# Performance work log

Measured on AMD Instinct MI355X. Metric: run time of the kernel, lower is better.

Reference implementation:

```python
import jax, jax.numpy as jnp
import numpy as np

# ---- config (mirrors init_kwargs) ----
T = 1024          # num tokens (one causal sequence)
H = 1024          # hidden_size
NQ, NK, D = 16, 4, 64   # q heads, kv heads, head_dim (GQA)
I_DENSE = 4096    # dense FFN intermediate
I_MOE = 512       # expert FFN intermediate
E, K = 8, 2       # num_experts, top_k
EPS = 1e-6
THETA = 10000.0


def setup_inputs() -> dict:
    key = jax.random.key(0)
    ks = jax.random.split(key, 20)
    rn = lambda k, shp: (jax.random.normal(k, shp, dtype=jnp.float32) * 0.02)
    QKV = (NQ + 2 * NK) * D
    return {
        "hidden_states": jax.random.normal(ks[0], (T, H), dtype=jnp.float32),
        "residual": jax.random.normal(ks[1], (T, H), dtype=jnp.float32),
        "positions": jnp.arange(T, dtype=jnp.int32),
        "ln0_w": jnp.ones((H,), jnp.float32),
        "pa0_w": jnp.ones((H,), jnp.float32),
        "ln1_w": jnp.ones((H,), jnp.float32),
        "pa1_w": jnp.ones((H,), jnp.float32),
        # attention weights (stored [in, out] so x @ W)
        "qkv0_w": rn(ks[2], (H, QKV)),
        "o0_w": rn(ks[3], (NQ * D, H)),
        "qkv1_w": rn(ks[4], (H, QKV)),
        "o1_w": rn(ks[5], (NQ * D, H)),
        # dense MLPs (merged gate_up: first half gate, second half up)
        "gu0_w": rn(ks[6], (H, 2 * I_DENSE)),
        "dn0_w": rn(ks[7], (I_DENSE, H)),
        "gu1_w": rn(ks[8], (H, 2 * I_DENSE)),
        "dn1_w": rn(ks[9], (I_DENSE, H)),
        # MoE: router gate + per-expert SwiGLU weights
        "gate_w": rn(ks[10], (H, E)),
        "w13": rn(ks[11], (E, H, 2 * I_MOE)),
        "w2": rn(ks[12], (E, I_MOE, H)),
    }


def _rmsnorm(x, w):
    v = jnp.mean(jnp.square(x.astype(jnp.float32)), axis=-1, keepdims=True)
    return (x.astype(jnp.float32) * jax.lax.rsqrt(v + EPS)).astype(x.dtype) * w


def _add_rmsnorm(x, res, w):
    # sglang fused add + RMSNorm: residual <- x + residual; out <- rmsnorm(residual)
    res = x + res
    return _rmsnorm(res, w), res


def _rope(pos, x):
    # neox-style rotary over full head_dim; x: [T, n_heads, D]
    half = D // 2
    inv_freq = 1.0 / (THETA ** (jnp.arange(half, dtype=jnp.float32) / half))
    f = pos.astype(jnp.float32)[:, None] * inv_freq            # [T, half]
    cos, sin = jnp.cos(f)[:, None, :], jnp.sin(f)[:, None, :]  # [T, 1, half]
    x1, x2 = x[..., :half], x[..., half:]
    return jnp.concatenate([x1 * cos - x2 * sin, x2 * cos + x1 * sin], axis=-1)


def _attention(pos, x, qkv_w, o_w):
    qkv = x @ qkv_w
    q = qkv[:, : NQ * D].reshape(T, NQ, D)
    k = qkv[:, NQ * D : (NQ + NK) * D].reshape(T, NK, D)
    v = qkv[:, (NQ + NK) * D :].reshape(T, NK, D)
    q, k = _rope(pos, q), _rope(pos, k)
    g = NQ // NK
    qg = q.reshape(T, NK, g, D)
    scores = jnp.einsum("tkgd,skd->kgts", qg, k) * (D ** -0.5)  # [NK,g,T,T]
    causal = jnp.tril(jnp.ones((T, T), bool))
    scores = jnp.where(causal, scores, jnp.float32(-1e30))
    p = jax.nn.softmax(scores, axis=-1)
    o = jnp.einsum("kgts,skd->tkgd", p, v).reshape(T, NQ * D)
    return o @ o_w


def _dense_mlp(x, gu_w, dn_w):
    gu = x @ gu_w
    h = jax.nn.silu(gu[:, :I_DENSE]) * gu[:, I_DENSE:]  # SiluAndMul
    return h @ dn_w


def _moe(x, gate_w, w13, w2):
    # router in fp32 (router_dtype == 'float32'), softmax, top-k, no renormalize
    logits = x.astype(jnp.float32) @ gate_w.astype(jnp.float32)  # [T, E]
    probs = jax.nn.softmax(logits, axis=-1)
    topw, topi = jax.lax.top_k(probs, K)                         # [T, K]
    rows = jnp.arange(x.shape[0])[:, None]
    combine = jnp.zeros((x.shape[0], E), jnp.float32).at[rows, topi].set(topw)
    combine = combine.astype(x.dtype)
    out = jnp.zeros_like(x)
    for e in range(E):  # fixed small expert count: grouped-GEMM reference
        g = x @ w13[e]
        h = jax.nn.silu(g[:, :I_MOE]) * g[:, I_MOE:]
        out = out + combine[:, e : e + 1] * (h @ w2[e])
    return out


def reference(hidden_states, residual, positions, ln0_w, pa0_w, ln1_w, pa1_w,
              qkv0_w, o0_w, qkv1_w, o1_w, gu0_w, dn0_w, gu1_w, dn1_w,
              gate_w, w13, w2):
    h, r = _add_rmsnorm(hidden_states, residual, ln0_w)
    h = _attention(positions, h, qkv0_w, o0_w)
    h, r = _add_rmsnorm(h, r, pa0_w)
    shortcut = _moe(h, gate_w, w13, w2)      # MoE runs on the shortcut branch
    h = _dense_mlp(h, gu0_w, dn0_w)
    h, r = _add_rmsnorm(h, r, ln1_w)
    h = _attention(positions, h, qkv1_w, o1_w)
    h, r = _add_rmsnorm(h, r, pa1_w)
    h = _dense_mlp(h, gu1_w, dn1_w)
    h = h + shortcut                          # combine shortcut MoE output
    return h, r
```

## Files before the change

kernel.cpp:

```cpp
#include <hip/hip_runtime.h>
#include <math.h>

namespace {

constexpr int kT = 1024;
constexpr int kH = 1024;
constexpr int kNQ = 16;
constexpr int kNKV = 4;
constexpr int kD = 64;
constexpr int kQKV = (kNQ + 2 * kNKV) * kD;
constexpr int kIDense = 4096;
constexpr int kIMoe = 512;
constexpr int kE = 8;
constexpr float kEps = 1e-6f;
constexpr long kTH = (long)kT * kH;

typedef __attribute__((ext_vector_type(8))) short short8;
typedef __attribute__((ext_vector_type(4))) float f32x4;

__device__ __forceinline__ ushort f2bf(float f) {
    union { float f; uint32_t u; } v; v.f = f;
    uint32_t r = (v.u + 0x7fffu + ((v.u >> 16) & 1u)) >> 16;
    return (ushort)r;
}
__device__ __forceinline__ void gload16(const void* g, void* l) {
    __builtin_amdgcn_global_load_lds(
        (const __attribute__((address_space(1))) void*)g,
        (__attribute__((address_space(3))) void*)l, 16, 0, 0);
}

__global__ __launch_bounds__(256) void add_rmsnorm_kernel(
    const float* __restrict__ xP, int nparts, const float* __restrict__ res,
    const float* __restrict__ w, float* __restrict__ h32,
    ushort* __restrict__ h16, float* __restrict__ r_out)
{
    __shared__ float red[4];
    const int t = blockIdx.x;
    const int i = threadIdx.x;
    const size_t base = (size_t)t * kH;
    float4 s = reinterpret_cast<const float4*>(res + base)[i];
    for (int p = 0; p < nparts; p++) {
        float4 a = reinterpret_cast<const float4*>(xP + p * kTH + base)[i];
        s.x += a.x; s.y += a.y; s.z += a.z; s.w += a.w;
    }
    reinterpret_cast<float4*>(r_out + base)[i] = s;
    float ss = s.x * s.x + s.y * s.y + s.z * s.z + s.w * s.w;
    #pragma unroll
    for (int off = 32; off > 0; off >>= 1) ss += __shfl_down(ss, off);
    if ((i & 63) == 0) red[i >> 6] = ss;
    __syncthreads();
    const float tot = red[0] + red[1] + red[2] + red[3];
    const float inv = rsqrtf(tot * (1.0f / kH) + kEps);
    float4 wv = reinterpret_cast<const float4*>(w)[i];
    float4 o = make_float4(s.x * inv * wv.x, s.y * inv * wv.y,
                           s.z * inv * wv.z, s.w * inv * wv.w);
    reinterpret_cast<float4*>(h32 + base)[i] = o;
    ushort4 u;
    u.x = f2bf(o.x); u.y = f2bf(o.y); u.z = f2bf(o.z); u.w = f2bf(o.w);
    reinterpret_cast<ushort4*>(h16 + base)[i] = u;
}

__global__ __launch_bounds__(256) void transpose_bf16_kernel(
    const float* __restrict__ W, ushort* __restrict__ WT,
    int R, int Cn, int ld_w, long w_z_stride, long wt_z_stride)
{
    __shared__ float tile[64 * 65];
    const int z = blockIdx.z;
    const float* Wz = W + (size_t)z * w_z_stride;
    ushort* WTz = WT + (size_t)z * wt_z_stride;
    const int r0 = blockIdx.y * 64;
    const int c0 = blockIdx.x * 64;
    const int tid = threadIdx.x;
    const int lr = tid >> 4;
    const int lc = (tid & 15) * 4;
    #pragma unroll
    for (int p = 0; p < 4; p++) {
        const int row = p * 16 + lr;
        float4 v = *reinterpret_cast<const float4*>(
            &Wz[(size_t)(r0 + row) * ld_w + c0 + lc]);
        tile[row * 65 + lc + 0] = v.x;
        tile[row * 65 + lc + 1] = v.y;
        tile[row * 65 + lc + 2] = v.z;
        tile[row * 65 + lc + 3] = v.w;
    }
    __syncthreads();
    const int ocl = tid >> 2;
    const int q = tid & 3;
    ushort u[16];
    #pragma unroll
    for (int e = 0; e < 16; e++)
        u[e] = f2bf(tile[(q * 16 + e) * 65 + ocl]);
    ushort* dst = &WTz[(size_t)(c0 + ocl) * R + r0 + q * 16];
    *reinterpret_cast<short8*>(dst) = *reinterpret_cast<short8*>(&u[0]);
    *reinterpret_cast<short8*>(dst + 8) = *reinterpret_cast<short8*>(&u[8]);
}

template <bool GATED>
__global__ __launch_bounds__(256) void mgemm_kernel(
    const ushort* __restrict__ A, const ushort* __restrict__ B,
    float* __restrict__ Cf, ushort* __restrict__ C16,
    const float* __restrict__ scale,
    int lda, int ldb, int ldc, int kc,
    int gate_off_rows, long b_z_stride, int c_z_col, int k_z_off,
    int scale_stride, long c_fstride)
{
    __shared__ __align__(16) ushort As[64 * 64];
    __shared__ __align__(16) ushort Bs[64 * 64];
    __shared__ __align__(16) ushort Us[GATED ? 64 * 64 : 8];

    const int z = blockIdx.z;
    const int gy = gridDim.y;
    const int nf = gridDim.x * gy;
    const int fid = blockIdx.x + gridDim.x * blockIdx.y;
    const int qq = nf >> 3;
    const int id2 = (fid & 7) * qq + (fid >> 3);
    const int m0 = (id2 % gy) * 64;
    const int n0 = (id2 / gy) * 64;

    const int tid = threadIdx.x;
    const ushort* Bz = B + (size_t)z * b_z_stride;
    const int k0 = z * k_z_off;

    const int arow = tid >> 3;
    const int achk = tid & 7;

    const int lane = tid & 63;
    const int wave = tid >> 6;
    const int wr = (wave >> 1) * 32;
    const int wc = (wave & 1) * 32;
    const int lrow = lane & 15;
    const int lg = lane >> 4;

    f32x4 accg[2][2] = {};
    f32x4 accu[2][2] = {};

    for (int kk0 = 0; kk0 < kc; kk0 += 64) {
        const int kbase = k0 + kk0;
        #pragma unroll
        for (int c = 0; c < 2; c++) {
            const int row = c * 32 + arow;
            const int cs = (achk + (row & 7)) & 7;
            gload16(A + (size_t)(m0 + row) * lda + kbase + cs * 8,
                    (char*)As + c * 4096 + tid * 16);
            gload16(Bz + (size_t)(n0 + row) * ldb + kbase + cs * 8,
                    (char*)Bs + c * 4096 + tid * 16);
            if constexpr (GATED)
                gload16(Bz + (size_t)(gate_off_rows + n0 + row) * ldb + kbase + cs * 8,
                        (char*)Us + c * 4096 + tid * 16);
        }
        __syncthreads();

        short8 af[2][2], bfr[2][2];
        #pragma unroll
        for (int mf = 0; mf < 2; mf++)
            #pragma unroll
            for (int kk = 0; kk < 2; kk++) {
                const int r = wr + mf * 16 + lrow;
                const int sl = ((kk * 4 + lg) - (r & 7)) & 7;
                af[mf][kk] = *reinterpret_cast<const short8*>(
                    (const char*)As + r * 128 + sl * 16);
            }
        #pragma unroll
        for (int nf2 = 0; nf2 < 2; nf2++)
            #pragma unroll
            for (int kk = 0; kk < 2; kk++) {
                const int n = wc + nf2 * 16 + lrow;
                const int sl = ((kk * 4 + lg) - (n & 7)) & 7;
                bfr[nf2][kk] = *reinterpret_cast<const short8*>(
                    (const char*)Bs + n * 128 + sl * 16);
            }
        #pragma unroll
        for (int mf = 0; mf < 2; mf++)
            #pragma unroll
            for (int nf2 = 0; nf2 < 2; nf2++)
                #pragma unroll
                for (int kk = 0; kk < 2; kk++)
                    accg[mf][nf2] = __builtin_amdgcn_mfma_f32_16x16x32_bf16(
                        af[mf][kk], bfr[nf2][kk], accg[mf][nf2], 0, 0, 0);
        if constexpr (GATED) {
            short8 uf[2][2];
            #pragma unroll
            for (int nf2 = 0; nf2 < 2; nf2++)
                #pragma unroll
                for (int kk = 0; kk < 2; kk++) {
                    const int n = wc + nf2 * 16 + lrow;
                    const int sl = ((kk * 4 + lg) - (n & 7)) & 7;
                    uf[nf2][kk] = *reinterpret_cast<const short8*>(
                        (const char*)Us + n * 128 + sl * 16);
                }
            #pragma unroll
            for (int mf = 0; mf < 2; mf++)
                #pragma unroll
                for (int nf2 = 0; nf2 < 2; nf2++)
                    #pragma unroll
                    for (int kk = 0; kk < 2; kk++)
                        accu[mf][nf2] = __builtin_amdgcn_mfma_f32_16x16x32_bf16(
                            af[mf][kk], uf[nf2][kk], accu[mf][nf2], 0, 0, 0);
        }
        __syncthreads();
    }

    const int r4 = (lane >> 4) * 4;
    const int cl = lane & 15;
    const int ccol = z * c_z_col;
    float* Cfz = Cf ? Cf + (size_t)z * c_fstride : nullptr;
    #pragma unroll
    for (int mf = 0; mf < 2; mf++) {
        #pragma unroll
        for (int nf2 = 0; nf2 < 2; nf2++) {
            #pragma unroll
            for (int j = 0; j < 4; j++) {
                const int row = m0 + wr + mf * 16 + r4 + j;
                const int col = ccol + n0 + wc + nf2 * 16 + cl;
                if constexpr (GATED) {
                    const float g = accg[mf][nf2][j];
                    const float u = accu[mf][nf2][j];
                    const float sv =
                        scale ? scale[(size_t)row * scale_stride + z] : 1.0f;
                    const float h = (g / (1.0f + __expf(-g))) * u * sv;
                    C16[(size_t)row * ldc + col] = f2bf(h);
                } else {
                    Cfz[(size_t)row * ldc + col] = accg[mf][nf2][j];
                }
            }
        }
    }
}

__global__ __launch_bounds__(256) void rope_pack_kernel(
    const float* __restrict__ qkv, const int* __restrict__ positions,
    ushort* __restrict__ Qb, ushort* __restrict__ Kb)
{
    const int t = blockIdx.x;
    const float pos = (float)positions[t];
    for (int item = threadIdx.x; item < (kNQ + kNKV) * 32; item += 256) {
        const int head = item >> 5;
        const int i = item & 31;
        const float inv_freq = powf(10000.0f, -(float)i * (1.0f / 32.0f));
        const float f = pos * inv_freq;
        float sv, cv;
        sincosf(f, &sv, &cv);
        const size_t off = (size_t)t * kQKV + head * kD;
        const float x1 = qkv[off + i];
        const float x2 = qkv[off + 32 + i];
        const float r1 = x1 * cv - x2 * sv;
        const float r2 = x2 * cv + x1 * sv;
        if (head < kNQ) {
            ushort* q = Qb + ((size_t)head * kT + t) * kD;
            q[i] = f2bf(r1 * 0.125f);
            q[i + 32] = f2bf(r2 * 0.125f);
        } else {
            ushort* k = Kb + ((size_t)(head - kNQ) * kT + t) * kD;
            k[i] = f2bf(r1);
            k[i + 32] = f2bf(r2);
        }
    }
}

__global__ __launch_bounds__(64) void gate_topk_kernel(
    const float* __restrict__ h, const float* __restrict__ gate_w,
    float* __restrict__ combine)
{
    const int t = blockIdx.x;
    const int lane = threadIdx.x;
    float acc[kE] = {};
    for (int i = lane; i < kH; i += 64) {
        const float xv = h[(size_t)t * kH + i];
        const float* gw = gate_w + (size_t)i * kE;
        #pragma unroll
        for (int e = 0; e < kE; e++) acc[e] += xv * gw[e];
    }
    #pragma unroll
    for (int e = 0; e < kE; e++) {
        #pragma unroll
        for (int off = 32; off > 0; off >>= 1) acc[e] += __shfl_down(acc[e], off);
    }
    if (lane == 0) {
        float mx = acc[0];
        #pragma unroll
        for (int e = 1; e < kE; e++) mx = fmaxf(mx, acc[e]);
        float p[kE];
        float s = 0.0f;
        #pragma unroll
        for (int e = 0; e < kE; e++) { p[e] = expf(acc[e] - mx); s += p[e]; }
        const float invs = 1.0f / s;
        #pragma unroll
        for (int e = 0; e < kE; e++) p[e] *= invs;
        int i1 = 0;
        #pragma unroll
        for (int e = 1; e < kE; e++) if (p[e] > p[i1]) i1 = e;
        int i2 = (i1 == 0) ? 1 : 0;
        #pragma unroll
        for (int e = 0; e < kE; e++) if (e != i1 && p[e] > p[i2]) i2 = e;
        float outv[kE];
        #pragma unroll
        for (int e = 0; e < kE; e++) outv[e] = 0.0f;
        outv[i1] = p[i1];
        outv[i2] = p[i2];
        #pragma unroll
        for (int e = 0; e < kE; e++) combine[(size_t)t * kE + e] = outv[e];
    }
}

__global__ __launch_bounds__(256) void attn_mfma_kernel(
    const ushort* __restrict__ Qb, const ushort* __restrict__ Kb,
    const ushort* __restrict__ Vt, float* __restrict__ Opart,
    float* __restrict__ mlpart)
{
    __shared__ __align__(16) ushort Qs[64 * 64];
    __shared__ __align__(16) ushort Ks[64 * 64];
    __shared__ __align__(16) ushort Vs[64 * 64];
    __shared__ __align__(16) ushort Ps[64 * 64];
    const int tid = threadIdx.x;
    const int qbi = (int)gridDim.x - 1 - blockIdx.x;
    const int qb = qbi * 64;
    const int hq = blockIdx.y;
    const int zp = blockIdx.z;
    const int kvh = hq >> 2;

    const int nt = qbi + 1;
    const int halfc = (nt + 1) >> 1;
    const int sbeg = zp ? halfc : 0;
    const int send = zp ? nt : halfc;

    float* Oz = Opart + (((size_t)zp * kNQ + hq) * kT + qb) * kD;
    float* mlz = mlpart + (((size_t)zp * kNQ + hq) * kT + qb) * 2;

    if (sbeg >= send) {
        for (int i = tid; i < 64 * kD; i += 256) Oz[(i >> 6) * kD + (i & 63)] = 0.f;
        for (int i = tid; i < 64; i += 256) { mlz[i * 2] = -1e30f; mlz[i * 2 + 1] = 0.f; }
        return;
    }

    const int lane = tid & 63;
    const int wave = tid >> 6;
    const int lrow = lane & 15;
    const int g = lane >> 4;
    const int srow = tid >> 3;
    const int sx = tid & 7;
    const ushort* Qg = Qb + ((size_t)hq * kT + qb) * kD;
    const ushort* Kg = Kb + (size_t)kvh * kT * kD;
    const ushort* Vg = Vt + (size_t)kvh * kD * kT;
    const int xr = (lrow & 7) << 4;

    #pragma unroll
    for (int c = 0; c < 2; c++) {
        const int row = c * 32 + srow;
        gload16(Qg + (size_t)row * kD + ((sx ^ (row & 7)) * 8),
                (char*)Qs + c * 4096 + tid * 16);
    }
    __syncthreads();
    short8 qf[2];
    #pragma unroll
    for (int kk = 0; kk < 2; kk++)
        qf[kk] = *reinterpret_cast<const short8*>(
            (const char*)Qs + (16 * wave + lrow) * 128 + ((kk * 64 + g * 16) ^ xr));

    f32x4 oacc[4] = {};
    float mrow = -1e30f, lsum = 0.0f;

    for (int ti = sbeg; ti < send; ++ti) {
        const int s0 = ti * 64;
        __syncthreads();
        #pragma unroll
        for (int c = 0; c < 2; c++) {
            const int row = c * 32 + srow;
            gload16(Kg + (size_t)(s0 + row) * kD + ((sx ^ (row & 7)) * 8),
                    (char*)Ks + c * 4096 + tid * 16);
            gload16(Vg + (size_t)row * kT + s0 + ((sx ^ (row & 7)) * 8),
                    (char*)Vs + c * 4096 + tid * 16);
        }
        __syncthreads();

        f32x4 sacc[4] = {};
        #pragma unroll
        for (int nf = 0; nf < 4; nf++) {
            #pragma unroll
            for (int kk = 0; kk < 2; kk++) {
                short8 kf = *reinterpret_cast<const short8*>(
                    (const char*)Ks + (nf * 16 + lrow) * 128 + ((kk * 64 + g * 16) ^ xr));
                sacc[nf] = __builtin_amdgcn_mfma_f32_16x16x32_bf16(
                    kf, qf[kk], sacc[nf], 0, 0, 0);
            }
        }

        const bool diag = (s0 == qb);
        float pv[16];
        float mloc = -1e30f;
        #pragma unroll
        for (int nf = 0; nf < 4; nf++)
            #pragma unroll
            for (int j = 0; j < 4; j++) {
                float s = sacc[nf][j];
                if (diag && (nf * 16 + g * 4 + j > 16 * wave + lrow)) s = -1e30f;
                pv[nf * 4 + j] = s;
                mloc = fmaxf(mloc, s);
            }
        mloc = fmaxf(mloc, __shfl_xor(mloc, 16));
        mloc = fmaxf(mloc, __shfl_xor(mloc, 32));
        const float mnew = fmaxf(mrow, mloc);
        const float alpha = __expf(mrow - mnew);
        float psum = 0.0f;
        #pragma unroll
        for (int j = 0; j < 16; j++) { pv[j] = __expf(pv[j] - mnew); psum += pv[j]; }
        psum += __shfl_xor(psum, 16);
        psum += __shfl_xor(psum, 32);
        lsum = lsum * alpha + psum;
        mrow = mnew;

        const int prow = 16 * wave + lrow;
        #pragma unroll
        for (int nf = 0; nf < 4; nf++)
            #pragma unroll
            for (int jp = 0; jp < 2; jp++) {
                uint32_t pk = (uint32_t)f2bf(pv[nf * 4 + jp * 2]) |
                              ((uint32_t)f2bf(pv[nf * 4 + jp * 2 + 1]) << 16);
                *reinterpret_cast<uint32_t*>(
                    (char*)Ps + prow * 128 + ((nf * 32 + g * 8 + jp * 4) ^ xr)) = pk;
            }

        float aj[4];
        #pragma unroll
        for (int j = 0; j < 4; j++) aj[j] = __shfl(alpha, g * 4 + j);
        #pragma unroll
        for (int nf = 0; nf < 4; nf++)
            #pragma unroll
            for (int j = 0; j < 4; j++) oacc[nf][j] *= aj[j];

        short8 paf[2];
        #pragma unroll
        for (int kk = 0; kk < 2; kk++)
            paf[kk] = *reinterpret_cast<const short8*>(
                (const char*)Ps + prow * 128 + ((kk * 64 + g * 16) ^ xr));
        #pragma unroll
        for (int nf = 0; nf < 4; nf++)
            #pragma unroll
            for (int kk = 0; kk < 2; kk++) {
                short8 vf = *reinterpret_cast<const short8*>(
                    (const char*)Vs + (nf * 16 + lrow) * 128 + ((kk * 64 + g * 16) ^ xr));
                oacc[nf] = __builtin_amdgcn_mfma_f32_16x16x32_bf16(
                    paf[kk], vf, oacc[nf], 0, 0, 0);
            }
    }

    #pragma unroll
    for (int nf = 0; nf < 4; nf++)
        #pragma unroll
        for (int j = 0; j < 4; j++)
            Oz[(16 * wave + g * 4 + j) * kD + nf * 16 + lrow] = oacc[nf][j];
    if (g == 0) {
        mlz[(16 * wave + lrow) * 2 + 0] = mrow;
        mlz[(16 * wave + lrow) * 2 + 1] = lsum;
    }
}

__global__ __launch_bounds__(256) void attn_merge_kernel(
    const float* __restrict__ Opart, const float* __restrict__ mlpart,
    ushort* __restrict__ attn_o)
{
    const int trow = blockIdx.x;
    const int tid = threadIdx.x;
    const int head = tid >> 4;
    const int c4 = (tid & 15) * 4;
    const size_t i0 = ((size_t)head * kT + trow);
    const size_t i1 = (((size_t)kNQ + head) * kT + trow);
    const float m0 = mlpart[i0 * 2], l0 = mlpart[i0 * 2 + 1];
    const float m1 = mlpart[i1 * 2], l1 = mlpart[i1 * 2 + 1];
    const float m = fmaxf(m0, m1);
    const float e0 = __expf(m0 - m), e1 = __expf(m1 - m);
    const float inv = 1.0f / (l0 * e0 + l1 * e1);
    float4 a = *reinterpret_cast<const float4*>(&Opart[i0 * kD + c4]);
    float4 b = *reinterpret_cast<const float4*>(&Opart[i1 * kD + c4]);
    ushort4 u;
    u.x = f2bf((a.x * e0 + b.x * e1) * inv);
    u.y = f2bf((a.y * e0 + b.y * e1) * inv);
    u.z = f2bf((a.z * e0 + b.z * e1) * inv);
    u.w = f2bf((a.w * e0 + b.w * e1) * inv);
    *reinterpret_cast<ushort4*>(
        &attn_o[(size_t)trow * (kNQ * kD) + head * kD + c4]) = u;
}

__global__ __launch_bounds__(256) void final_out_kernel(
    const float* __restrict__ mlpP, const float* __restrict__ scP,
    const float* __restrict__ r, float* __restrict__ out)
{
    const int i = blockIdx.x * 256 + threadIdx.x;
    float4 s = make_float4(0.f, 0.f, 0.f, 0.f);
    #pragma unroll
    for (int p = 0; p < 4; p++) {
        float4 a = reinterpret_cast<const float4*>(mlpP + p * kTH)[i];
        float4 b = reinterpret_cast<const float4*>(scP + p * kTH)[i];
        s.x += a.x + b.x; s.y += a.y + b.y; s.z += a.z + b.z; s.w += a.w + b.w;
    }
    reinterpret_cast<float4*>(out)[i] = s;
    reinterpret_cast<float4*>(out + kTH)[i] =
        reinterpret_cast<const float4*>(r)[i];
}

}

extern "C" void kernel_launch(void* const* d_in, const int* in_sizes, int n_in,
                              void* d_out, int out_size, void* d_ws, size_t ws_size,
                              hipStream_t stream) {
    (void)in_sizes; (void)n_in; (void)out_size; (void)ws_size;
    const float* hidden   = (const float*)d_in[0];
    const float* residual = (const float*)d_in[1];
    const int*   positions= (const int*)d_in[2];
    const float* ln0_w    = (const float*)d_in[3];
    const float* pa0_w    = (const float*)d_in[4];
    const float* ln1_w    = (const float*)d_in[5];
    const float* pa1_w    = (const float*)d_in[6];
    const float* qkv0_w   = (const float*)d_in[7];
    const float* o0_w     = (const float*)d_in[8];
    const float* qkv1_w   = (const float*)d_in[9];
    const float* o1_w     = (const float*)d_in[10];
    const float* gu0_w    = (const float*)d_in[11];
    const float* dn0_w    = (const float*)d_in[12];
    const float* gu1_w    = (const float*)d_in[13];
    const float* dn1_w    = (const float*)d_in[14];
    const float* gate_w   = (const float*)d_in[15];
    const float* w13      = (const float*)d_in[16];
    const float* w2       = (const float*)d_in[17];
    float* out_h = (float*)d_out;

    char* wsb = (char*)d_ws;
    float*  r_buf   = (float*)(wsb + (0ull  << 20));
    float*  h32     = (float*)(wsb + (4ull  << 20));
    float*  t0P     = (float*)(wsb + (8ull  << 20));
    float*  cb_buf  = (float*)(wsb + (8ull  << 20));
    float*  Opart   = (float*)(wsb + (16ull << 20));
    float*  scP     = (float*)(wsb + (24ull << 20));
    ushort* h16     = (ushort*)(wsb + (40ull << 20));
    ushort* ao16    = (ushort*)(wsb + (42ull << 20));
    float*  qkv_buf = (float*)(wsb + (44ull << 20));
    ushort* he16    = (ushort*)(wsb + (44ull << 20));
    float*  ml_buf  = (float*)(wsb + (50ull << 20));
    ushort* wT      = (ushort*)(wsb + (52ull << 20));
    ushort* Qb      = (ushort*)(wsb + (62ull << 20));
    ushort* Kb      = (ushort*)(wsb + (64ull << 20));
    ushort* VtG     = (ushort*)(wsb + (65ull << 20));

    auto transp = [&](const float* W, int R, int Cn, int nz, long zs_in, long zs_out) {
        transpose_bf16_kernel<<<dim3(Cn / 64, R / 64, nz), 256, 0, stream>>>(
            W, wT, R, Cn, Cn, zs_in, zs_out);
    };
    auto gemm_f32 = [&](const ushort* A, float* C, int N, int lda_,
                        int ldb_, int ldc_, int nz, int kc, int kzoff) {
        mgemm_kernel<false><<<dim3(N / 64, kT / 64, nz), 256, 0, stream>>>(
            A, wT, C, nullptr, nullptr, lda_, ldb_, ldc_, kc,
            0, 0, 0, kzoff, 0, kTH);
    };
    auto attention = [&](const float* qkv_w, const float* o_w) {
        transp(qkv_w, kH, kQKV, 1, 0, 0);
        mgemm_kernel<false><<<dim3(kQKV / 64, kT / 64, 1), 256, 0, stream>>>(
            h16, wT, qkv_buf, nullptr, nullptr, kH, kH, kQKV, kH,
            0, 0, 0, 0, 0, 0);
        rope_pack_kernel<<<kT, 256, 0, stream>>>(qkv_buf, positions, Qb, Kb);
        transpose_bf16_kernel<<<dim3(1, kT / 64, kNKV), 256, 0, stream>>>(
            qkv_buf + (kNQ + kNKV) * kD, VtG, kT, kD, kQKV, kD, (long)kD * kT);
        attn_mfma_kernel<<<dim3(kT / 64, kNQ, 2), 256, 0, stream>>>(
            Qb, Kb, VtG, Opart, ml_buf);
        attn_merge_kernel<<<kT, 256, 0, stream>>>(Opart, ml_buf, ao16);
        transp(o_w, kNQ * kD, kH, 1, 0, 0);
        gemm_f32(ao16, t0P, kH, kNQ * kD, kNQ * kD, kH, 2, 512, 512);
    };
    auto dense_mlp = [&](const float* gu_w, const float* dn_w) {
        transp(gu_w, kH, 2 * kIDense, 1, 0, 0);
        mgemm_kernel<true><<<dim3(kIDense / 64, kT / 64, 1), 256, 0, stream>>>(
            h16, wT, nullptr, he16, nullptr, kH, kH, kIDense, kH,
            kIDense, 0, 0, 0, 0, 0);
        transp(dn_w, kIDense, kH, 1, 0, 0);
        gemm_f32(he16, t0P, kH, kIDense, kIDense, kH, 4, 1024, 1024);
    };

    add_rmsnorm_kernel<<<kT, 256, 0, stream>>>(hidden, 1, residual, ln0_w, h32, h16, r_buf);
    attention(qkv0_w, o0_w);
    add_rmsnorm_kernel<<<kT, 256, 0, stream>>>(t0P, 2, r_buf, pa0_w, h32, h16, r_buf);
    gate_topk_kernel<<<kT, 64, 0, stream>>>(h32, gate_w, cb_buf);
    transp(w13, kH, 2 * kIMoe, kE, (long)kH * 2 * kIMoe, (long)kH * 2 * kIMoe);
    mgemm_kernel<true><<<dim3(kIMoe / 64, kT / 64, kE), 256, 0, stream>>>(
        h16, wT, nullptr, he16, cb_buf, kH, kH, kIDense, kH,
        kIMoe, (long)kH * 2 * kIMoe, kIMoe, 0, kE, 0);
    transp(w2, kE * kIMoe, kH, 1, 0, 0);
    gemm_f32(he16, scP, kH, kIDense, kIDense, kH, 4, 1024, 1024);
    dense_mlp(gu0_w, dn0_w);
    add_rmsnorm_kernel<<<kT, 256, 0, stream>>>(t0P, 4, r_buf, ln1_w, h32, h16, r_buf);
    attention(qkv1_w, o1_w);
    add_rmsnorm_kernel<<<kT, 256, 0, stream>>>(t0P, 2, r_buf, pa1_w, h32, h16, r_buf);
    dense_mlp(gu1_w, dn1_w);
    final_out_kernel<<<(kT * kH / 4) / 256, 256, 0, stream>>>(t0P, scP, r_buf, out_h);
}
```

Before: 335.8 us.

## Widen GEMM tiles to 64x128 with 512 threads and fuse router into RMSNorm

Replaces the 64x64 MFMA GEMM with a 64x128 tile variant run by 8 waves, so each A tile loaded into LDS is reused across twice as many output columns and the block count halves. Separately, the MoE router logits, softmax and top-2 selection are folded into the post-attention add+RMSNorm kernel, removing one launch and a reread of the normalized activations. The larger tile doubles LDS use per block and reduces grid size, which may cut occupancy on small GEMMs such as the MoE ones.

```diff
diff --git a/kernel.cpp b/kernel.cpp
--- a/kernel.cpp
+++ b/kernel.cpp
@@ -32,9 +32,11 @@
 __global__ __launch_bounds__(256) void add_rmsnorm_kernel(
     const float* __restrict__ xP, int nparts, const float* __restrict__ res,
     const float* __restrict__ w, float* __restrict__ h32,
-    ushort* __restrict__ h16, float* __restrict__ r_out)
+    ushort* __restrict__ h16, float* __restrict__ r_out,
+    const float* __restrict__ gate_w, float* __restrict__ combine)
 {
     __shared__ float red[4];
+    __shared__ float gred[4][kE];
     const int t = blockIdx.x;
     const int i = threadIdx.x;
     const size_t base = (size_t)t * kH;
@@ -58,6 +60,51 @@
     ushort4 u;
     u.x = f2bf(o.x); u.y = f2bf(o.y); u.z = f2bf(o.z); u.w = f2bf(o.w);
     reinterpret_cast<ushort4*>(h16 + base)[i] = u;
+
+    if (gate_w != nullptr) {
+        float le[kE];
+        const float* gw = gate_w + (size_t)(i * 4) * kE;
+        #pragma unroll
+        for (int e = 0; e < kE; e++)
+            le[e] = o.x * gw[e] + o.y * gw[kE + e] +
+                    o.z * gw[2 * kE + e] + o.w * gw[3 * kE + e];
+        #pragma unroll
+        for (int e = 0; e < kE; e++) {
+            #pragma unroll
+            for (int off = 32; off > 0; off >>= 1)
+                le[e] += __shfl_down(le[e], off);
+        }
+        if ((i & 63) == 0) {
+            #pragma unroll
+            for (int e = 0; e < kE; e++) gred[i >> 6][e] = le[e];
+        }
+        __syncthreads();
+        if (i == 0) {
+            float p[kE];
+            float mx = -1e30f;
+            #pragma unroll
+            for (int e = 0; e < kE; e++) {
+                p[e] = gred[0][e] + gred[1][e] + gred[2][e] + gred[3][e];
+                mx = fmaxf(mx, p[e]);
+            }
+            float sum = 0.0f;
+            #pragma unroll
+            for (int e = 0; e < kE; e++) { p[e] = __expf(p[e] - mx); sum += p[e]; }
+            const float invs = 1.0f / sum;
+            #pragma unroll
+            for (int e = 0; e < kE; e++) p[e] *= invs;
+            int i1 = 0;
+            #pragma unroll
+            for (int e = 1; e < kE; e++) if (p[e] > p[i1]) i1 = e;
+            int i2 = (i1 == 0) ? 1 : 0;
+            #pragma unroll
+            for (int e = 0; e < kE; e++) if (e != i1 && p[e] > p[i2]) i2 = e;
+            #pragma unroll
+            for (int e = 0; e < kE; e++)
+                combine[(size_t)t * kE + e] =
+                    (e == i1) ? p[i1] : (e == i2) ? p[i2] : 0.0f;
+        }
+    }
 }
 
 __global__ __launch_bounds__(256) void transpose_bf16_kernel(
@@ -96,7 +143,7 @@
 }
 
 template <bool GATED>
-__global__ __launch_bounds__(256) void mgemm_kernel(
+__global__ __launch_bounds__(512) void mgemm128_kernel(
     const ushort* __restrict__ A, const ushort* __restrict__ B,
     float* __restrict__ Cf, ushort* __restrict__ C16,
     const float* __restrict__ scale,
@@ -105,8 +152,8 @@
     int scale_stride, long c_fstride)
 {
     __shared__ __align__(16) ushort As[64 * 64];
-    __shared__ __align__(16) ushort Bs[64 * 64];
-    __shared__ __align__(16) ushort Us[GATED ? 64 * 64 : 8];
+    __shared__ __align__(16) ushort Bs[128 * 64];
+    __shared__ __align__(16) ushort Us[GATED ? 128 * 64 : 8];
 
     const int z = blockIdx.z;
     const int gy = gridDim.y;
@@ -115,19 +162,19 @@
     const int qq = nf >> 3;
     const int id2 = (fid & 7) * qq + (fid >> 3);
     const int m0 = (id2 % gy) * 64;
-    const int n0 = (id2 / gy) * 64;
+    const int n0 = (id2 / gy) * 128;
 
     const int tid = threadIdx.x;
     const ushort* Bz = B + (size_t)z * b_z_stride;
     const int k0 = z * k_z_off;
 
-    const int arow = tid >> 3;
-    const int achk = tid & 7;
+    const int sr = tid >> 3;
+    const int sc = tid & 7;
 
     const int lane = tid & 63;
     const int wave = tid >> 6;
-    const int wr = (wave >> 1) * 32;
-    const int wc = (wave & 1) * 32;
+    const int wr = (wave >> 2) * 32;
+    const int wc = (wave & 3) * 32;
     const int lrow = lane & 15;
     const int lg = lane >> 4;
 
@@ -136,17 +183,20 @@
 
     for (int kk0 = 0; kk0 < kc; kk0 += 64) {
         const int kbase = k0 + kk0;
+        {
+            const int csA = (sc + (sr & 7)) & 7;
+            gload16(A + (size_t)(m0 + sr) * lda + kbase + csA * 8,
+                    (char*)As + tid * 16);
+        }
         #pragma unroll
         for (int c = 0; c < 2; c++) {
-            const int row = c * 32 + arow;
-            const int cs = (achk + (row & 7)) & 7;
-            gload16(A + (size_t)(m0 + row) * lda + kbase + cs * 8,
-                    (char*)As + c * 4096 + tid * 16);
+            const int row = c * 64 + sr;
+            const int cs = (sc + (row & 7)) & 7;
             gload16(Bz + (size_t)(n0 + row) * ldb + kbase + cs * 8,
-                    (char*)Bs + c * 4096 + tid * 16);
+                    (char*)Bs + c * 8192 + tid * 16);
             if constexpr (GATED)
                 gload16(Bz + (size_t)(gate_off_rows + n0 + row) * ldb + kbase + cs * 8,
-                        (char*)Us + c * 4096 + tid * 16);
+                        (char*)Us + c * 8192 + tid * 16);
         }
         __syncthreads();
 
@@ -257,51 +307,6 @@
     }
 }
 
-__global__ __launch_bounds__(64) void gate_topk_kernel(
-    const float* __restrict__ h, const float* __restrict__ gate_w,
-    float* __restrict__ combine)
-{
-    const int t = blockIdx.x;
-    const int lane = threadIdx.x;
-    float acc[kE] = {};
-    for (int i = lane; i < kH; i += 64) {
-        const float xv = h[(size_t)t * kH + i];
-        const float* gw = gate_w + (size_t)i * kE;
-        #pragma unroll
-        for (int e = 0; e < kE; e++) acc[e] += xv * gw[e];
-    }
-    #pragma unroll
-    for (int e = 0; e < kE; e++) {
-        #pragma unroll
-        for (int off = 32; off > 0; off >>= 1) acc[e] += __shfl_down(acc[e], off);
-    }
-    if (lane == 0) {
-        float mx = acc[0];
-        #pragma unroll
-        for (int e = 1; e < kE; e++) mx = fmaxf(mx, acc[e]);
-        float p[kE];
-        float s = 0.0f;
-        #pragma unroll
-        for (int e = 0; e < kE; e++) { p[e] = expf(acc[e] - mx); s += p[e]; }
-        const float invs = 1.0f / s;
-        #pragma unroll
-        for (int e = 0; e < kE; e++) p[e] *= invs;
-        int i1 = 0;
-        #pragma unroll
-        for (int e = 1; e < kE; e++) if (p[e] > p[i1]) i1 = e;
-        int i2 = (i1 == 0) ? 1 : 0;
-        #pragma unroll
-        for (int e = 0; e < kE; e++) if (e != i1 && p[e] > p[i2]) i2 = e;
-        float outv[kE];
-        #pragma unroll
-        for (int e = 0; e < kE; e++) outv[e] = 0.0f;
-        outv[i1] = p[i1];
-        outv[i2] = p[i2];
-        #pragma unroll
-        for (int e = 0; e < kE; e++) combine[(size_t)t * kE + e] = outv[e];
-    }
-}
-
 __global__ __launch_bounds__(256) void attn_mfma_kernel(
     const ushort* __restrict__ Qb, const ushort* __restrict__ Kb,
     const ushort* __restrict__ Vt, float* __restrict__ Opart,
@@ -544,15 +549,14 @@
         transpose_bf16_kernel<<<dim3(Cn / 64, R / 64, nz), 256, 0, stream>>>(
             W, wT, R, Cn, Cn, zs_in, zs_out);
     };
-    auto gemm_f32 = [&](const ushort* A, float* C, int N, int lda_,
-                        int ldb_, int ldc_, int nz, int kc, int kzoff) {
-        mgemm_kernel<false><<<dim3(N / 64, kT / 64, nz), 256, 0, stream>>>(
-            A, wT, C, nullptr, nullptr, lda_, ldb_, ldc_, kc,
-            0, 0, 0, kzoff, 0, kTH);
+    auto rmsnorm = [&](const float* xP, int nparts, const float* wn,
+                       const float* gw, float* cb) {
+        add_rmsnorm_kernel<<<kT, 256, 0, stream>>>(
+            xP, nparts, r_buf, wn, h32, h16, r_buf, gw, cb);
     };
     auto attention = [&](const float* qkv_w, const float* o_w) {
         transp(qkv_w, kH, kQKV, 1, 0, 0);
-        mgemm_kernel<false><<<dim3(kQKV / 64, kT / 64, 1), 256, 0, stream>>>(
+        mgemm128_kernel<false><<<dim3(kQKV / 128, kT / 64, 1), 512, 0, stream>>>(
             h16, wT, qkv_buf, nullptr, nullptr, kH, kH, kQKV, kH,
             0, 0, 0, 0, 0, 0);
         rope_pack_kernel<<<kT, 256, 0, stream>>>(qkv_buf, positions, Qb, Kb);
@@ -562,31 +566,37 @@
             Qb, Kb, VtG, Opart, ml_buf);
         attn_merge_kernel<<<kT, 256, 0, stream>>>(Opart, ml_buf, ao16);
         transp(o_w, kNQ * kD, kH, 1, 0, 0);
-        gemm_f32(ao16, t0P, kH, kNQ * kD, kNQ * kD, kH, 2, 512, 512);
+        mgemm128_kernel<false><<<dim3(kH / 128, kT / 64, 2), 512, 0, stream>>>(
+            ao16, wT, t0P, nullptr, nullptr, kNQ * kD, kNQ * kD, kH, 512,
+            0, 0, 0, 512, 0, kTH);
     };
     auto dense_mlp = [&](const float* gu_w, const float* dn_w) {
         transp(gu_w, kH, 2 * kIDense, 1, 0, 0);
-        mgemm_kernel<true><<<dim3(kIDense / 64, kT / 64, 1), 256, 0, stream>>>(
+        mgemm128_kernel<true><<<dim3(kIDense / 128, kT / 64, 1), 512, 0, stream>>>(
             h16, wT, nullptr, he16, nullptr, kH, kH, kIDense, kH,
             kIDense, 0, 0, 0, 0, 0);
         transp(dn_w, kIDense, kH, 1, 0, 0);
-        gemm_f32(he16, t0P, kH, kIDense, kIDense, kH, 4, 1024, 1024);
+        mgemm128_kernel<false><<<dim3(kH / 128, kT / 64, 4), 512, 0, stream>>>(
+            he16, wT, t0P, nullptr, nullptr, kIDense, kIDense, kH, 1024,
+            0, 0, 0, 1024, 0, kTH);
     };
 
-    add_rmsnorm_kernel<<<kT, 256, 0, stream>>>(hidden, 1, residual, ln0_w, h32, h16, r_buf);
+    add_rmsnorm_kernel<<<kT, 256, 0, stream>>>(
+        hidden, 1, residual, ln0_w, h32, h16, r_buf, nullptr, nullptr);
     attention(qkv0_w, o0_w);
-    add_rmsnorm_kernel<<<kT, 256, 0, stream>>>(t0P, 2, r_buf, pa0_w, h32, h16, r_buf);
-    gate_topk_kernel<<<kT, 64, 0, stream>>>(h32, gate_w, cb_buf);
+    rmsnorm(t0P, 2, pa0_w, gate_w, cb_buf);
     transp(w13, kH, 2 * kIMoe, kE, (long)kH * 2 * kIMoe, (long)kH * 2 * kIMoe);
-    mgemm_kernel<true><<<dim3(kIMoe / 64, kT / 64, kE), 256, 0, stream>>>(
+    mgemm128_kernel<true><<<dim3(kIMoe / 128, kT / 64, kE), 512, 0, stream>>>(
         h16, wT, nullptr, he16, cb_buf, kH, kH, kIDense, kH,
         kIMoe, (long)kH * 2 * kIMoe, kIMoe, 0, kE, 0);
     transp(w2, kE * kIMoe, kH, 1, 0, 0);
-    gemm_f32(he16, scP, kH, kIDense, kIDense, kH, 4, 1024, 1024);
+    mgemm128_kernel<false><<<dim3(kH / 128, kT / 64, 4), 512, 0, stream>>>(
+        he16, wT, scP, nullptr, nullptr, kIDense, kIDense, kH, 1024,
+        0, 0, 0, 1024, 0, kTH);
     dense_mlp(gu0_w, dn0_w);
-    add_rmsnorm_kernel<<<kT, 256, 0, stream>>>(t0P, 4, r_buf, ln1_w, h32, h16, r_buf);
+    rmsnorm(t0P, 4, ln1_w, nullptr, nullptr);
     attention(qkv1_w, o1_w);
-    add_rmsnorm_kernel<<<kT, 256, 0, stream>>>(t0P, 2, r_buf, pa1_w, h32, h16, r_buf);
+    rmsnorm(t0P, 2, pa1_w, nullptr, nullptr);
     dense_mlp(gu1_w, dn1_w);
     final_out_kernel<<<(kT * kH / 4) / 256, 256, 0, stream>>>(t0P, scP, r_buf, out_h);
 }
```

Measured after the change: 319.2 us. -4.9%, faster.
